# Kernel optimization log

Measured on AMD Instinct MI355X. Metric: run time of the kernel, lower is better.

## Reference

```python
import jax, jax.numpy as jnp
import numpy as np

N_NODES = 50000
N_EDGES = 312500
IN_F = 256
OUT_F = 256


def setup_inputs() -> dict:
    key = jax.random.key(0)
    kx, ki, kj, kw, kb = jax.random.split(key, 5)
    x = jax.random.normal(kx, (N_NODES, IN_F), dtype=jnp.float32)
    Ai = jax.random.randint(ki, (N_EDGES,), 0, N_NODES, dtype=jnp.int64)
    Aj = jax.random.randint(kj, (N_EDGES,), 0, N_NODES, dtype=jnp.int64)
    # Linear(2*in_features, out_features): PyTorch default uniform(-1/sqrt(fan_in), 1/sqrt(fan_in))
    bound = 1.0 / np.sqrt(2 * IN_F)
    W = jax.random.uniform(kw, (OUT_F, 2 * IN_F), dtype=jnp.float32, minval=-bound, maxval=bound)
    b = jax.random.uniform(kb, (OUT_F,), dtype=jnp.float32, minval=-bound, maxval=bound)
    return {"x": x, "W": W, "b": b, "Ai": Ai, "Aj": Aj}


def reference(x, W, b, Ai, Aj):
    X_i = x[Ai]                      # [E, F] gather source rows
    X_j = x[Aj]                      # [E, F]
    X_ij = jnp.concatenate([X_i, X_j], axis=1)   # [E, 2F]
    E_msg = jnp.einsum('ef,of->eo', X_ij, W) + b  # [E, out]
    agg_xi = jax.ops.segment_sum(E_msg, Ai, num_segments=N_NODES)  # [N, out]
    return agg_xi
```

## Files before the change

kernel.cpp:

```cpp
#include <hip/hip_runtime.h>
#include <hip/hip_bf16.h>

#define NN 50000
#define NE 312500
#define FIN 256
#define NT 1564
#define CAP 64

typedef __attribute__((ext_vector_type(4))) float f32x4;
typedef __attribute__((ext_vector_type(2))) float f32x2;
typedef __attribute__((ext_vector_type(8))) short bf16x8;
typedef __attribute__((ext_vector_type(4))) unsigned short u16x4;
typedef __attribute__((ext_vector_type(8))) unsigned short u16x8;
typedef __attribute__((ext_vector_type(4))) unsigned int u32x4;

#ifndef __has_builtin
#define __has_builtin(x) 0
#endif
#if __has_builtin(__builtin_amdgcn_cvt_pk_f32_fp8) && __has_builtin(__builtin_amdgcn_cvt_pk_fp8_f32)
#define HWFP8 1
#else
#define HWFP8 0
#endif

__device__ __forceinline__ float bf2f(unsigned short u) {
  return __builtin_bit_cast(float, ((unsigned int)u) << 16);
}
__device__ __forceinline__ unsigned short f2bf(float f) {
  return __builtin_bit_cast(unsigned short, __float2bfloat16(f));
}

#if !HWFP8
__device__ __forceinline__ unsigned enc8(float f) {
  unsigned bits = __builtin_bit_cast(unsigned, f);
  unsigned s = bits >> 31;
  unsigned a = bits & 0x7FFFFFFFu;
  if (a < 0x3C400000u) return s << 7;
  a += 0x0007FFFFu + ((a >> 20) & 1);
  unsigned e = (a >> 23) - 120u;
  unsigned m = (a >> 20) & 7u;
  if (e > 15u) { e = 15u; m = 6u; }
  return (s << 7) | (e << 3) | m;
}
__device__ __forceinline__ float dec8(unsigned b) {
  unsigned s = (b >> 7) & 1u, e = (b >> 3) & 15u, m = b & 7u;
  float v = e ? __builtin_bit_cast(float, ((e + 120u) << 23) | (m << 20))
              : (float)m * 0.001953125f;
  return s ? -v : v;
}
#endif

__device__ __forceinline__ unsigned enc4fp8(float a, float b, float c, float d) {
#if HWFP8
  int pk = __builtin_amdgcn_cvt_pk_fp8_f32(a, b, 0, false);
  pk = __builtin_amdgcn_cvt_pk_fp8_f32(c, d, pk, true);
  return (unsigned)pk;
#else
  return enc8(a) | (enc8(b) << 8) | (enc8(c) << 16) | (enc8(d) << 24);
#endif
}

__device__ __forceinline__ void dec4fp8(unsigned w, float* r) {
#if HWFP8
  f32x2 lo = __builtin_amdgcn_cvt_pk_f32_fp8((int)w, false);
  f32x2 hi = __builtin_amdgcn_cvt_pk_f32_fp8((int)w, true);
  r[0] = lo[0]; r[1] = lo[1]; r[2] = hi[0]; r[3] = hi[1];
#else
  r[0] = dec8(w & 255); r[1] = dec8((w >> 8) & 255);
  r[2] = dec8((w >> 16) & 255); r[3] = dec8(w >> 24);
#endif
}

__device__ __forceinline__ bf16x8 cvt8v(f32x4 a, f32x4 b) {
  bf16x8 r;
  #pragma unroll
  for (int i = 0; i < 4; ++i) {
    r[i]     = (short)f2bf(a[i]);
    r[i + 4] = (short)f2bf(b[i]);
  }
  return r;
}

__device__ __forceinline__ bf16x8 cvt8(const float* p) {
  return cvt8v(*(const f32x4*)p, *(const f32x4*)(p + 4));
}

__global__ __launch_bounds__(256) void k_wz(const float* __restrict__ W,
                                            unsigned short* __restrict__ WbP,
                                            int* __restrict__ deg) {
  if (blockIdx.x >= 64) {
    int i = (blockIdx.x - 64) * 256 + threadIdx.x;
    if (i < 50048) deg[i] = 0;
    return;
  }
  int lane = threadIdx.x & 63, wid = threadIdx.x >> 6;
  int c = blockIdx.x * 4 + wid;
  int o16 = c >> 3, kk = c & 7;
  int lr = lane & 15, lk = lane >> 4;
  int o = o16 * 16 + lr;
  int k = kk * 32 + lk * 8;
  const float* src = (o < 256) ? (W + (size_t)o * 512 + k)
                               : (W + (size_t)(o - 256) * 512 + 256 + k);
  *(bf16x8*)(WbP + (size_t)c * 512 + lane * 8) = cvt8(src);
}

__global__ __launch_bounds__(512) void k_gemm(
    const float* __restrict__ x, const unsigned short* __restrict__ WbP,
    unsigned short* __restrict__ Y1b, unsigned char* __restrict__ Y2f8,
    const int* __restrict__ Ai, const int* __restrict__ Aj,
    int* __restrict__ deg, int* __restrict__ edst) {
  __shared__ __align__(16) unsigned short A[2][8192];
  const int tid = threadIdx.x;
  const int lane = tid & 63, w = tid >> 6;
  const int lr = lane & 15, lk = lane >> 4;

  const int row0 = (tid >> 5);
  const int seg = tid & 31;
  const int uoff0 = ((row0 >> 4) * 8 + (seg >> 2)) * 512 +
                    (((((seg & 3) * 16) + (row0 & 15)) * 8) ^ ((seg & 7) << 3));
  const int row1 = 16 + row0;
  const int uoff1 = ((row1 >> 4) * 8 + (seg >> 2)) * 512 +
                    (((((seg & 3) * 16) + (row1 & 15)) * 8) ^ ((seg & 7) << 3));

  f32x4 pa, pb, pc, pd;
  {
    int g0 = blockIdx.x * 32 + row0; if (g0 > NN - 1) g0 = NN - 1;
    int g1 = blockIdx.x * 32 + row1; if (g1 > NN - 1) g1 = NN - 1;
    const float* s0 = x + (size_t)g0 * FIN + seg * 8;
    const float* s1 = x + (size_t)g1 * FIN + seg * 8;
    pa = *(const f32x4*)s0; pb = *(const f32x4*)(s0 + 4);
    pc = *(const f32x4*)s1; pd = *(const f32x4*)(s1 + 4);
  }

  for (int e = blockIdx.x * 512 + tid; e < NE; e += 256 * 512) {
    int a = Ai[e];
    int p = atomicAdd(&deg[a], 1);
    edst[a * CAP + p] = Aj[e];
  }

  bf16x8 B[8][4];
  #pragma unroll
  for (int kk = 0; kk < 8; ++kk)
    #pragma unroll
    for (int n = 0; n < 4; ++n)
      B[kk][n] = *(const bf16x8*)(WbP + ((size_t)(w * 4 + n) * 8 + kk) * 512 + lane * 8);
  #pragma unroll
  for (int kk = 0; kk < 8; ++kk)
    #pragma unroll
    for (int n = 0; n < 4; ++n)
      asm volatile("" : "+v"(B[kk][n]));

  *(bf16x8*)(&A[0][uoff0]) = cvt8v(pa, pb);
  *(bf16x8*)(&A[0][uoff1]) = cvt8v(pc, pd);
  __syncthreads();

  int p = 0;
  for (int tile = blockIdx.x; tile < NT; tile += 256) {
    const int nxt = tile + 256;
    const bool hn = (nxt < NT);

    f32x4 a0, b0, a1, b1;
    if (hn) {
      int g0 = nxt * 32 + row0; if (g0 > NN - 1) g0 = NN - 1;
      int g1 = nxt * 32 + row1; if (g1 > NN - 1) g1 = NN - 1;
      const float* s0 = x + (size_t)g0 * FIN + seg * 8;
      const float* s1 = x + (size_t)g1 * FIN + seg * 8;
      a0 = *(const f32x4*)s0; b0 = *(const f32x4*)(s0 + 4);
      a1 = *(const f32x4*)s1; b1 = *(const f32x4*)(s1 + 4);
    }

    f32x4 acc[2][4];
    #pragma unroll
    for (int rg = 0; rg < 2; ++rg)
      #pragma unroll
      for (int n = 0; n < 4; ++n) acc[rg][n] = (f32x4){0.f, 0.f, 0.f, 0.f};
    #pragma unroll
    for (int rg = 0; rg < 2; ++rg) {
      #pragma unroll
      for (int kk = 0; kk < 8; ++kk) {
        bf16x8 af = *(const bf16x8*)(
            &A[p][(rg * 8 + kk) * 512 + ((lane * 8) ^ (((kk & 1) << 5) | (lk << 3)))]);
        #pragma unroll
        for (int n = 0; n < 4; ++n)
          acc[rg][n] = __builtin_amdgcn_mfma_f32_16x16x32_bf16(af, B[kk][n], acc[rg][n], 0, 0, 0);
      }
    }

    #pragma unroll
    for (int rg = 0; rg < 2; ++rg) {
      #pragma unroll
      for (int rr = 0; rr < 4; ++rr) {
        int row = tile * 32 + rg * 16 + lk * 4 + rr;
        if (w < 4) {
          u16x4 v;
          #pragma unroll
          for (int n = 0; n < 4; ++n)
            v[n] = f2bf(acc[rg][n][rr]);
          *(u16x4*)(Y1b + (size_t)row * 256 + w * 64 + lr * 4) = v;
        } else {
          unsigned pk = enc4fp8(acc[rg][0][rr], acc[rg][1][rr],
                                acc[rg][2][rr], acc[rg][3][rr]);
          *(unsigned int*)(Y2f8 + (size_t)row * 256 + (w - 4) * 64 + lr * 4) = pk;
        }
      }
    }

    if (hn) {
      *(bf16x8*)(&A[p ^ 1][uoff0]) = cvt8v(a0, b0);
      *(bf16x8*)(&A[p ^ 1][uoff1]) = cvt8v(a1, b1);
      __syncthreads();
    }
    p ^= 1;
  }
}

__global__ __launch_bounds__(256) void k_epi(
    const unsigned short* __restrict__ Y1b, const unsigned char* __restrict__ Y2f8,
    const int* __restrict__ deg, const int* __restrict__ edst,
    const float* __restrict__ bias, float* __restrict__ out) {
  __shared__ float sm[2048];
  int wid = threadIdx.x >> 6;
  int lane = threadIdx.x & 63;
  int half = lane >> 5;
  int es = (lane >> 4) & 1;
  int fg = lane & 15;
  int base = blockIdx.x * 8 + wid * 2;
  int n = base + half;
  int o = n * CAP;
  int c = deg[n];

  u16x8 y10 = *(const u16x8*)(Y1b + (size_t)n * 256 + fg * 16);
  u16x8 y11 = *(const u16x8*)(Y1b + (size_t)n * 256 + fg * 16 + 8);

  const unsigned char* Y2 = Y2f8 + fg * 16;
  f32x4 ac[4];
  #pragma unroll
  for (int h = 0; h < 4; ++h) ac[h] = (f32x4){0.f, 0.f, 0.f, 0.f};

  int e = es;
  for (; e + 2 < c; e += 4) {
    int jA = edst[o + e];
    int jB = edst[o + e + 2];
    u32x4 vA = *(const u32x4*)(Y2 + (size_t)jA * 256);
    u32x4 vB = *(const u32x4*)(Y2 + (size_t)jB * 256);
    #pragma unroll
    for (int h = 0; h < 4; ++h) {
      float rA[4], rB[4];
      dec4fp8(vA[h], rA);
      dec4fp8(vB[h], rB);
      #pragma unroll
      for (int i = 0; i < 4; ++i) ac[h][i] += rA[i] + rB[i];
    }
  }
  if (e < c) {
    int j = edst[o + e];
    u32x4 v = *(const u32x4*)(Y2 + (size_t)j * 256);
    #pragma unroll
    for (int h = 0; h < 4; ++h) {
      float r[4];
      dec4fp8(v[h], r);
      #pragma unroll
      for (int i = 0; i < 4; ++i) ac[h][i] += r[i];
    }
  }

  #pragma unroll
  for (int h = 0; h < 4; ++h)
    #pragma unroll
    for (int i = 0; i < 4; ++i)
      ac[h][i] += __shfl_xor(ac[h][i], 16);

  float* Wm = sm + (wid * 2 + half) * 256;
  if (es == 0) {
    float dg = (float)c;
    #pragma unroll
    for (int i = 0; i < 16; ++i) {
      int p = fg * 16 + i;
      int tc = (p & ~63) | ((p & 3) << 4) | ((p >> 2) & 15);
      float y1 = bf2f((i < 8) ? y10[i] : y11[i - 8]);
      Wm[tc] = dg * (y1 + bias[tc]) + ac[i >> 2][i & 3];
    }
  }
  asm volatile("s_waitcnt lgkmcnt(0)" ::: "memory");
  #pragma unroll
  for (int h = 0; h < 2; ++h) {
    f32x4 res = *(const f32x4*)(sm + (wid * 2 + h) * 256 + lane * 4);
    __builtin_nontemporal_store(res, (f32x4*)out + (size_t)(base + h) * 64 + lane);
  }
}

extern "C" void kernel_launch(void* const* d_in, const int* in_sizes, int n_in,
                              void* d_out, int out_size, void* d_ws, size_t ws_size,
                              hipStream_t stream) {
  const float* x = (const float*)d_in[0];
  const float* W = (const float*)d_in[1];
  const float* b = (const float*)d_in[2];
  const int* Ai = (const int*)d_in[3];
  const int* Aj = (const int*)d_in[4];
  float* out = (float*)d_out;

  int* ip = (int*)d_ws;
  int* deg  = ip;
  int* edst = ip + 50048;
  unsigned short* WbP  = (unsigned short*)(ip + 3253120);
  unsigned short* Y1b  = (unsigned short*)(ip + 3318656);
  unsigned char*  Y2f8 = (unsigned char*)(ip + 9724800);

  k_wz<<<260, 256, 0, stream>>>(W, WbP, deg);
  k_gemm<<<256, 512, 0, stream>>>(x, WbP, Y1b, Y2f8, Ai, Aj, deg, edst);
  k_epi<<<6250, 256, 0, stream>>>(Y1b, Y2f8, deg, edst, b, out);
}
```

Before: 69.62 us.

## Pre-convert x to packed bf16 and stage W half in LDS per block

Adds a prepass in the first kernel that converts x to bf16 in the MFMA fragment layout, so the GEMM reads A fragments straight from global memory without fp32 loads, conversion or LDS double buffering. Each GEMM block now owns one output family (Y1 or Y2) and loads that half of the packed W into 128KB of LDS via global_load_lds. Each wave then handles whole 32-row tiles across all 256 columns. This removes per-tile barriers and in-GEMM conversion, but adds an extra write and read pass over a bf16 copy of x and makes every x tile be read twice, once per family.

```diff
diff --git a/kernel.cpp b/kernel.cpp
--- a/kernel.cpp
+++ b/kernel.cpp
@@ -85,51 +85,55 @@
   return cvt8v(*(const f32x4*)p, *(const f32x4*)(p + 4));
 }
 
-__global__ __launch_bounds__(256) void k_wz(const float* __restrict__ W,
-                                            unsigned short* __restrict__ WbP,
-                                            int* __restrict__ deg) {
-  if (blockIdx.x >= 64) {
-    int i = (blockIdx.x - 64) * 256 + threadIdx.x;
+__global__ __launch_bounds__(256) void k_wzx(const float* __restrict__ W,
+                                             unsigned short* __restrict__ WbP,
+                                             int* __restrict__ deg,
+                                             const float* __restrict__ x,
+                                             unsigned short* __restrict__ xbP) {
+  int b = blockIdx.x;
+  int lane = threadIdx.x & 63, wid = threadIdx.x >> 6;
+  if (b < 64) {
+    int c = b * 4 + wid;
+    int o16 = c >> 3, kk = c & 7;
+    int lr = lane & 15, lk = lane >> 4;
+    int o = o16 * 16 + lr;
+    int k = kk * 32 + lk * 8;
+    const float* src = (o < 256) ? (W + (size_t)o * 512 + k)
+                                 : (W + (size_t)(o - 256) * 512 + 256 + k);
+    *(bf16x8*)(WbP + (size_t)c * 512 + lane * 8) = cvt8(src);
+  } else if (b < 260) {
+    int i = (b - 64) * 256 + threadIdx.x;
     if (i < 50048) deg[i] = 0;
-    return;
-  }
-  int lane = threadIdx.x & 63, wid = threadIdx.x >> 6;
-  int c = blockIdx.x * 4 + wid;
-  int o16 = c >> 3, kk = c & 7;
-  int lr = lane & 15, lk = lane >> 4;
-  int o = o16 * 16 + lr;
-  int k = kk * 32 + lk * 8;
-  const float* src = (o < 256) ? (W + (size_t)o * 512 + k)
-                               : (W + (size_t)(o - 256) * 512 + 256 + k);
-  *(bf16x8*)(WbP + (size_t)c * 512 + lane * 8) = cvt8(src);
+  } else {
+    int c = (b - 260) * 4 + wid;
+    int row = (c >> 3) * 16 + (lane & 15);
+    int k0 = (c & 7) * 32 + (lane >> 4) * 8;
+    bf16x8 v = {0, 0, 0, 0, 0, 0, 0, 0};
+    if (row < NN) v = cvt8(x + (size_t)row * FIN + k0);
+    *(bf16x8*)(xbP + (size_t)c * 512 + lane * 8) = v;
+  }
 }
 
 __global__ __launch_bounds__(512) void k_gemm(
-    const float* __restrict__ x, const unsigned short* __restrict__ WbP,
+    const unsigned short* __restrict__ xbP, const unsigned short* __restrict__ WbP,
     unsigned short* __restrict__ Y1b, unsigned char* __restrict__ Y2f8,
     const int* __restrict__ Ai, const int* __restrict__ Aj,
     int* __restrict__ deg, int* __restrict__ edst) {
-  __shared__ __align__(16) unsigned short A[2][8192];
+  __shared__ __align__(16) unsigned short Blds[65536];
   const int tid = threadIdx.x;
   const int lane = tid & 63, w = tid >> 6;
   const int lr = lane & 15, lk = lane >> 4;
-
-  const int row0 = (tid >> 5);
-  const int seg = tid & 31;
-  const int uoff0 = ((row0 >> 4) * 8 + (seg >> 2)) * 512 +
-                    (((((seg & 3) * 16) + (row0 & 15)) * 8) ^ ((seg & 7) << 3));
-  const int row1 = 16 + row0;
-  const int uoff1 = ((row1 >> 4) * 8 + (seg >> 2)) * 512 +
-                    (((((seg & 3) * 16) + (row1 & 15)) * 8) ^ ((seg & 7) << 3));
-
-  f32x4 pa, pb, pc, pd;
-  {
-    int g0 = blockIdx.x * 32 + row0; if (g0 > NN - 1) g0 = NN - 1;
-    int g1 = blockIdx.x * 32 + row1; if (g1 > NN - 1) g1 = NN - 1;
-    const float* s0 = x + (size_t)g0 * FIN + seg * 8;
-    const float* s1 = x + (size_t)g1 * FIN + seg * 8;
-    pa = *(const f32x4*)s0; pb = *(const f32x4*)(s0 + 4);
-    pc = *(const f32x4*)s1; pd = *(const f32x4*)(s1 + 4);
+  const int fam = blockIdx.x & 1;
+  const int bf_id = blockIdx.x >> 1;
+
+  #pragma unroll
+  for (int i = 0; i < 16; ++i) {
+    int ch = w * 16 + i;
+    __builtin_amdgcn_global_load_lds(
+        (const __attribute__((address_space(1))) void*)(
+            WbP + ((size_t)(fam * 128 + ch)) * 512 + lane * 8),
+        (__attribute__((address_space(3))) void*)(Blds + ch * 512 + lane * 8),
+        16, 0, 0);
   }
 
   for (int e = blockIdx.x * 512 + tid; e < NE; e += 256 * 512) {
@@ -138,79 +142,56 @@
     edst[a * CAP + p] = Aj[e];
   }
 
-  bf16x8 B[8][4];
-  #pragma unroll
-  for (int kk = 0; kk < 8; ++kk)
-    #pragma unroll
-    for (int n = 0; n < 4; ++n)
-      B[kk][n] = *(const bf16x8*)(WbP + ((size_t)(w * 4 + n) * 8 + kk) * 512 + lane * 8);
-  #pragma unroll
-  for (int kk = 0; kk < 8; ++kk)
-    #pragma unroll
-    for (int n = 0; n < 4; ++n)
-      asm volatile("" : "+v"(B[kk][n]));
-
-  *(bf16x8*)(&A[0][uoff0]) = cvt8v(pa, pb);
-  *(bf16x8*)(&A[0][uoff1]) = cvt8v(pc, pd);
   __syncthreads();
 
-  int p = 0;
-  for (int tile = blockIdx.x; tile < NT; tile += 256) {
-    const int nxt = tile + 256;
-    const bool hn = (nxt < NT);
-
-    f32x4 a0, b0, a1, b1;
-    if (hn) {
-      int g0 = nxt * 32 + row0; if (g0 > NN - 1) g0 = NN - 1;
-      int g1 = nxt * 32 + row1; if (g1 > NN - 1) g1 = NN - 1;
-      const float* s0 = x + (size_t)g0 * FIN + seg * 8;
-      const float* s1 = x + (size_t)g1 * FIN + seg * 8;
-      a0 = *(const f32x4*)s0; b0 = *(const f32x4*)(s0 + 4);
-      a1 = *(const f32x4*)s1; b1 = *(const f32x4*)(s1 + 4);
-    }
-
-    f32x4 acc[2][4];
+  for (int tile = bf_id * 8 + w; tile < NT; tile += 1024) {
+    bf16x8 af[2][8];
     #pragma unroll
     for (int rg = 0; rg < 2; ++rg)
       #pragma unroll
-      for (int n = 0; n < 4; ++n) acc[rg][n] = (f32x4){0.f, 0.f, 0.f, 0.f};
-    #pragma unroll
-    for (int rg = 0; rg < 2; ++rg) {
+      for (int kk = 0; kk < 8; ++kk)
+        af[rg][kk] = *(const bf16x8*)(
+            xbP + ((size_t)(tile * 2 + rg) * 8 + kk) * 512 + lane * 8);
+
+    #pragma unroll
+    for (int cg = 0; cg < 4; ++cg) {
+      f32x4 acc[2][4];
+      #pragma unroll
+      for (int rg = 0; rg < 2; ++rg)
+        #pragma unroll
+        for (int c = 0; c < 4; ++c) acc[rg][c] = (f32x4){0.f, 0.f, 0.f, 0.f};
       #pragma unroll
       for (int kk = 0; kk < 8; ++kk) {
-        bf16x8 af = *(const bf16x8*)(
-            &A[p][(rg * 8 + kk) * 512 + ((lane * 8) ^ (((kk & 1) << 5) | (lk << 3)))]);
-        #pragma unroll
-        for (int n = 0; n < 4; ++n)
-          acc[rg][n] = __builtin_amdgcn_mfma_f32_16x16x32_bf16(af, B[kk][n], acc[rg][n], 0, 0, 0);
+        bf16x8 Bf[4];
+        #pragma unroll
+        for (int c = 0; c < 4; ++c)
+          Bf[c] = *(const bf16x8*)(Blds + ((cg * 4 + c) * 8 + kk) * 512 + lane * 8);
+        #pragma unroll
+        for (int rg = 0; rg < 2; ++rg)
+          #pragma unroll
+          for (int c = 0; c < 4; ++c)
+            acc[rg][c] = __builtin_amdgcn_mfma_f32_16x16x32_bf16(
+                af[rg][kk], Bf[c], acc[rg][c], 0, 0, 0);
       }
-    }
-
-    #pragma unroll
-    for (int rg = 0; rg < 2; ++rg) {
-      #pragma unroll
-      for (int rr = 0; rr < 4; ++rr) {
-        int row = tile * 32 + rg * 16 + lk * 4 + rr;
-        if (w < 4) {
-          u16x4 v;
-          #pragma unroll
-          for (int n = 0; n < 4; ++n)
-            v[n] = f2bf(acc[rg][n][rr]);
-          *(u16x4*)(Y1b + (size_t)row * 256 + w * 64 + lr * 4) = v;
-        } else {
-          unsigned pk = enc4fp8(acc[rg][0][rr], acc[rg][1][rr],
-                                acc[rg][2][rr], acc[rg][3][rr]);
-          *(unsigned int*)(Y2f8 + (size_t)row * 256 + (w - 4) * 64 + lr * 4) = pk;
+      #pragma unroll
+      for (int rg = 0; rg < 2; ++rg) {
+        #pragma unroll
+        for (int rr = 0; rr < 4; ++rr) {
+          int row = tile * 32 + rg * 16 + lk * 4 + rr;
+          if (fam == 0) {
+            u16x4 v;
+            #pragma unroll
+            for (int c = 0; c < 4; ++c)
+              v[c] = f2bf(acc[rg][c][rr]);
+            *(u16x4*)(Y1b + (size_t)row * 256 + cg * 64 + lr * 4) = v;
+          } else {
+            unsigned pk = enc4fp8(acc[rg][0][rr], acc[rg][1][rr],
+                                  acc[rg][2][rr], acc[rg][3][rr]);
+            *(unsigned int*)(Y2f8 + (size_t)row * 256 + cg * 64 + lr * 4) = pk;
+          }
         }
       }
     }
-
-    if (hn) {
-      *(bf16x8*)(&A[p ^ 1][uoff0]) = cvt8v(a0, b0);
-      *(bf16x8*)(&A[p ^ 1][uoff1]) = cvt8v(a1, b1);
-      __syncthreads();
-    }
-    p ^= 1;
   }
 }
 
@@ -305,8 +286,9 @@
   unsigned short* WbP  = (unsigned short*)(ip + 3253120);
   unsigned short* Y1b  = (unsigned short*)(ip + 3318656);
   unsigned char*  Y2f8 = (unsigned char*)(ip + 9724800);
-
-  k_wz<<<260, 256, 0, stream>>>(W, WbP, deg);
-  k_gemm<<<256, 512, 0, stream>>>(x, WbP, Y1b, Y2f8, Ai, Aj, deg, edst);
+  unsigned short* xbP  = (unsigned short*)(ip + 12927872);
+
+  k_wzx<<<6516, 256, 0, stream>>>(W, WbP, deg, x, xbP);
+  k_gemm<<<256, 512, 0, stream>>>(xbP, WbP, Y1b, Y2f8, Ai, Aj, deg, edst);
   k_epi<<<6250, 256, 0, stream>>>(Y1b, Y2f8, deg, edst, b, out);
 }
```

New measurement: 198.9 us. 186% more time.
